# Kernel optimization log

Measured on AMD Instinct MI355X. Metric: run time of the kernel, lower is better.

The kernel has to match this reference:

```python
import jax, jax.numpy as jnp
import numpy as np

TEMPERATURE = 8.0


def setup_inputs() -> dict:
    key = jax.random.key(0)
    kq, kk, kv, kc = jax.random.split(key, 4)
    B, L, D = 4, 4096, 64
    q = jax.random.normal(kq, (B, L, D), dtype=jnp.float32)
    k = jax.random.normal(kk, (B, L, D), dtype=jnp.float32)
    v = jax.random.normal(kv, (B, L, D), dtype=jnp.float32)
    # vectors = stack(softmax(randn(d_v)), softmax(randn(d_v)))  (dim=0 softmax over d_v)
    raw = jax.random.normal(kc, (2, D), dtype=jnp.float32)
    vectors = jax.nn.softmax(raw, axis=1)
    return {"q": q, "k": k, "v": v, "vectors": vectors}


def reference(q, k, v, vectors):
    # Original builds diagonal core tensors cores[t,t,t] = vectors[.,t] for t < min(dimen, len_q),
    # then einsum('pqk,bip,bjq,bkr->bijr') and sums over j. With a diagonal core this collapses to:
    #   out[b,i,r] = sum_{t<m} q[b,i,t] * w[t] * ksum[b,t] * v[b,t,r]
    # where w = 0.5*(c1+c2)/temperature and ksum[b,t] = sum_j k[b,j,t].
    B, L, D = q.shape
    m = min(D, L)  # static python int
    w = 0.5 * (vectors[0, :m] + vectors[1, :m]) / TEMPERATURE          # [m]
    ksum = jnp.sum(k[:, :, :m], axis=1)                                 # [B, m]
    coef = w[None, :] * ksum                                            # [B, m]
    output = jnp.einsum('bit,bt,btr->bir', q[:, :, :m], coef, v[:, :m, :])  # [B, L, D]
    attn = jnp.einsum('bid,bjd->bij', q, k)                             # [B, L, L]
    return (output, attn)
```

## Files before the change

kernel.cpp:

```cpp
#include <hip/hip_runtime.h>
#include <stdint.h>

#define BB 4
#define LL 4096
#define DD 64

typedef __attribute__((ext_vector_type(8))) short bf16x8;
typedef __attribute__((ext_vector_type(4))) float f32x4;

static __device__ __forceinline__ unsigned short f2bf(float x) {
    unsigned int u = __builtin_bit_cast(unsigned int, x);
    u += 0x7fffu + ((u >> 16) & 1u);
    return (unsigned short)(u >> 16);
}

__global__ __launch_bounds__(256) void convert_kernel(
    const float* __restrict__ q, const float* __restrict__ k,
    unsigned short* __restrict__ qbf, unsigned short* __restrict__ kbf,
    float* __restrict__ part)
{
    const int NBQ = (BB * LL * DD) / 2048;
    int bid = blockIdx.x;
    bool is_k = bid >= NBQ;
    const float* src = is_k ? k : q;
    unsigned short* dst = is_k ? kbf : qbf;
    int cb = is_k ? (bid - NBQ) : bid;
    int tid = threadIdx.x;

    size_t idx0 = (size_t)cb * 2048 + (size_t)tid * 8;
    float4 f0 = *(const float4*)(src + idx0);
    float4 f1 = *(const float4*)(src + idx0 + 4);
    float f[8] = {f0.x, f0.y, f0.z, f0.w, f1.x, f1.y, f1.z, f1.w};

    unsigned short u[8];
    #pragma unroll
    for (int e = 0; e < 8; e++) u[e] = f2bf(f[e]);
    uint4 pk;
    pk.x = (unsigned)u[0] | ((unsigned)u[1] << 16);
    pk.y = (unsigned)u[2] | ((unsigned)u[3] << 16);
    pk.z = (unsigned)u[4] | ((unsigned)u[5] << 16);
    pk.w = (unsigned)u[6] | ((unsigned)u[7] << 16);
    *(uint4*)(dst + idx0) = pk;

    if (is_k) {
        __shared__ float red[256][8];
        #pragma unroll
        for (int e = 0; e < 8; e++) red[tid][e] = f[e];
        __syncthreads();
        if (tid < 64) {
            int g = tid >> 3, e = tid & 7;
            float s = 0.f;
            #pragma unroll
            for (int r = 0; r < 32; r++) s += red[r * 8 + g][e];
            part[(size_t)cb * 64 + tid] = s;
        }
    }
}

__global__ __launch_bounds__(256) void out_kernel(
    const float* __restrict__ q, const float* __restrict__ v,
    const float* __restrict__ vec, const float* __restrict__ part,
    float* __restrict__ out)
{
    __shared__ float csh[64];
    __shared__ float Vl[64][65];
    __shared__ float qs[32][65];

    int bid = blockIdx.x;
    int b   = bid >> 7;
    int i0  = (bid & 127) << 5;
    int tid = threadIdx.x;

    if (tid < 64) {
        const float* pp = part + (size_t)b * 128 * 64 + tid;
        float s = 0.f;
        #pragma unroll 8
        for (int c = 0; c < 128; c++) s += pp[c * 64];
        csh[tid] = 0.0625f * (vec[tid] + vec[64 + tid]) * s;
    }
    {
        const float* vb = v + (size_t)b * LL * DD;
        #pragma unroll
        for (int it = 0; it < 4; it++) {
            int idx4 = it * 256 + tid;
            int t  = idx4 >> 4;
            int r4 = (idx4 & 15) << 2;
            float4 w = *(const float4*)(vb + (size_t)idx4 * 4);
            Vl[t][r4 + 0] = w.x; Vl[t][r4 + 1] = w.y;
            Vl[t][r4 + 2] = w.z; Vl[t][r4 + 3] = w.w;
        }
    }
    __syncthreads();
    {
        const float* qb = q + (size_t)b * LL * DD;
        int row = tid >> 3;
        int t0  = (tid & 7) << 3;
        const float* src = qb + (size_t)(i0 + row) * DD + t0;
        float4 a0 = *(const float4*)(src);
        float4 a1 = *(const float4*)(src + 4);
        float fa[8] = {a0.x,a0.y,a0.z,a0.w,a1.x,a1.y,a1.z,a1.w};
        #pragma unroll
        for (int e = 0; e < 8; e++) qs[row][t0 + e] = fa[e] * csh[t0 + e];
    }
    __syncthreads();

    int ii = tid >> 3;
    int g  = tid & 7;
    float acc[8] = {0,0,0,0,0,0,0,0};
    #pragma unroll 8
    for (int t = 0; t < 64; t++) {
        float qv = qs[ii][t];
        #pragma unroll
        for (int j = 0; j < 8; j++) acc[j] += qv * Vl[t][g * 8 + j];
    }
    float* op = out + (size_t)b * LL * DD + (size_t)(i0 + ii) * DD + g * 8;
    float4 s0 = {acc[0], acc[1], acc[2], acc[3]};
    float4 s1 = {acc[4], acc[5], acc[6], acc[7]};
    *(float4*)(op)     = s0;
    *(float4*)(op + 4) = s1;
}

__global__ __launch_bounds__(256) void attn_kernel(
    const unsigned short* __restrict__ qbf,
    const unsigned short* __restrict__ kbf,
    float* __restrict__ attn)
{
    int bid = blockIdx.x;
    int swz = (bid & 7) * 512 + (bid >> 3);
    int b   = swz >> 10;
    int rem = swz & 1023;
    int ti  = rem >> 5;
    int tj  = rem & 31;

    int tid  = threadIdx.x;
    int wid  = tid >> 6;
    int lane = tid & 63;
    int wm = wid >> 1, wn = wid & 1;
    int row0 = ti * 128 + wm * 64;
    int col0 = tj * 128 + wn * 64;

    const unsigned short* qb = qbf + (size_t)b * LL * DD;
    const unsigned short* kb = kbf + (size_t)b * LL * DD;

    int lr = lane & 15;
    int lk = (lane >> 4) * 8;

    f32x4 acc[4][4];
    #pragma unroll
    for (int m = 0; m < 4; m++)
        #pragma unroll
        for (int n = 0; n < 4; n++)
            acc[m][n] = (f32x4){0.f, 0.f, 0.f, 0.f};

    #pragma unroll
    for (int kk = 0; kk < 2; kk++) {
        int k0 = kk * 32 + lk;
        bf16x8 qf[4], kf[4];
        #pragma unroll
        for (int m = 0; m < 4; m++)
            qf[m] = *(const bf16x8*)(qb + (size_t)(row0 + m * 16 + lr) * DD + k0);
        #pragma unroll
        for (int n = 0; n < 4; n++)
            kf[n] = *(const bf16x8*)(kb + (size_t)(col0 + n * 16 + lr) * DD + k0);
        #pragma unroll
        for (int m = 0; m < 4; m++)
            #pragma unroll
            for (int n = 0; n < 4; n++)
                acc[m][n] = __builtin_amdgcn_mfma_f32_16x16x32_bf16(
                    kf[n], qf[m], acc[m][n], 0, 0, 0);
    }

    float* ab = attn + (size_t)b * LL * LL;
    int jb = (lane >> 4) * 4;
    #pragma unroll
    for (int m = 0; m < 4; m++) {
        size_t roff = (size_t)(row0 + m * 16 + lr) * LL;
        #pragma unroll
        for (int n = 0; n < 4; n++) {
            *(f32x4*)(ab + roff + col0 + n * 16 + jb) = acc[m][n];
        }
    }
}

extern "C" void kernel_launch(void* const* d_in, const int* in_sizes, int n_in,
                              void* d_out, int out_size, void* d_ws, size_t ws_size,
                              hipStream_t stream) {
    const float* q   = (const float*)d_in[0];
    const float* k   = (const float*)d_in[1];
    const float* v   = (const float*)d_in[2];
    const float* vec = (const float*)d_in[3];

    float* out  = (float*)d_out;
    float* attn = out + (size_t)BB * LL * DD;

    unsigned short* qbf = (unsigned short*)d_ws;
    unsigned short* kbf = qbf + (size_t)BB * LL * DD;
    float* part = (float*)(kbf + (size_t)BB * LL * DD);

    convert_kernel<<<1024, 256, 0, stream>>>(q, k, qbf, kbf, part);
    out_kernel<<<512, 256, 0, stream>>>(q, v, vec, part, out);
    attn_kernel<<<4096, 256, 0, stream>>>(qbf, kbf, attn);
}
```

Measured before the change: 81.03 us.

## Stage attn tiles through swizzled LDS for fully coalesced row stores

The attn kernel now gives each block a 32x512 output tile instead of 128x128, with each wave computing 32x128. Results are written into an XOR-swizzled LDS buffer and then stored to global memory as contiguous 2KB row segments. Previously each lane wrote scattered 16-byte pieces across many rows. The aim is better write coalescing on the store-bound 256MB attn output, at the cost of 64KB of LDS per block, which limits occupancy, plus an extra LDS round trip and a barrier.

```diff
diff --git a/kernel.cpp b/kernel.cpp
--- a/kernel.cpp
+++ b/kernel.cpp
@@ -125,60 +125,74 @@
     const unsigned short* __restrict__ kbf,
     float* __restrict__ attn)
 {
+    __shared__ float lds[32 * 512];
+
     int bid = blockIdx.x;
     int swz = (bid & 7) * 512 + (bid >> 3);
     int b   = swz >> 10;
     int rem = swz & 1023;
-    int ti  = rem >> 5;
-    int tj  = rem & 31;
+    int ti  = rem >> 3;
+    int tj  = rem & 7;
 
     int tid  = threadIdx.x;
     int wid  = tid >> 6;
     int lane = tid & 63;
-    int wm = wid >> 1, wn = wid & 1;
-    int row0 = ti * 128 + wm * 64;
-    int col0 = tj * 128 + wn * 64;
+    int i0 = ti * 32;
+    int j0 = tj * 512;
+    int jw = j0 + wid * 128;
 
     const unsigned short* qb = qbf + (size_t)b * LL * DD;
     const unsigned short* kb = kbf + (size_t)b * LL * DD;
 
     int lr = lane & 15;
-    int lk = (lane >> 4) * 8;
-
-    f32x4 acc[4][4];
-    #pragma unroll
-    for (int m = 0; m < 4; m++)
-        #pragma unroll
-        for (int n = 0; n < 4; n++)
+    int g  = lane >> 4;
+    int lk = g * 8;
+
+    f32x4 acc[2][8];
+    #pragma unroll
+    for (int m = 0; m < 2; m++)
+        #pragma unroll
+        for (int n = 0; n < 8; n++)
             acc[m][n] = (f32x4){0.f, 0.f, 0.f, 0.f};
 
     #pragma unroll
     for (int kk = 0; kk < 2; kk++) {
         int k0 = kk * 32 + lk;
-        bf16x8 qf[4], kf[4];
-        #pragma unroll
-        for (int m = 0; m < 4; m++)
-            qf[m] = *(const bf16x8*)(qb + (size_t)(row0 + m * 16 + lr) * DD + k0);
-        #pragma unroll
-        for (int n = 0; n < 4; n++)
-            kf[n] = *(const bf16x8*)(kb + (size_t)(col0 + n * 16 + lr) * DD + k0);
-        #pragma unroll
-        for (int m = 0; m < 4; m++)
+        bf16x8 qf[2], kf[8];
+        #pragma unroll
+        for (int m = 0; m < 2; m++)
+            qf[m] = *(const bf16x8*)(qb + (size_t)(i0 + m * 16 + lr) * DD + k0);
+        #pragma unroll
+        for (int n = 0; n < 8; n++)
+            kf[n] = *(const bf16x8*)(kb + (size_t)(jw + n * 16 + lr) * DD + k0);
+        #pragma unroll
+        for (int m = 0; m < 2; m++)
             #pragma unroll
-            for (int n = 0; n < 4; n++)
+            for (int n = 0; n < 8; n++)
                 acc[m][n] = __builtin_amdgcn_mfma_f32_16x16x32_bf16(
                     kf[n], qf[m], acc[m][n], 0, 0, 0);
     }
 
+    f32x4* l4 = (f32x4*)lds;
+    #pragma unroll
+    for (int m = 0; m < 2; m++) {
+        int row = m * 16 + lr;
+        #pragma unroll
+        for (int n = 0; n < 8; n++) {
+            int col4 = wid * 32 + n * 4 + g;
+            l4[row * 128 + (col4 ^ (row & 7))] = acc[m][n];
+        }
+    }
+    __syncthreads();
+
     float* ab = attn + (size_t)b * LL * LL;
-    int jb = (lane >> 4) * 4;
-    #pragma unroll
-    for (int m = 0; m < 4; m++) {
-        size_t roff = (size_t)(row0 + m * 16 + lr) * LL;
-        #pragma unroll
-        for (int n = 0; n < 4; n++) {
-            *(f32x4*)(ab + roff + col0 + n * 16 + jb) = acc[m][n];
-        }
+    #pragma unroll
+    for (int it = 0; it < 16; it++) {
+        int flat4 = it * 256 + tid;
+        int row   = flat4 >> 7;
+        int col4  = flat4 & 127;
+        f32x4 v = l4[row * 128 + (col4 ^ (row & 7))];
+        *(f32x4*)(ab + (size_t)(i0 + row) * LL + j0 + col4 * 4) = v;
     }
 }
 
```

Result: faster. 78.47 us (-3.2%).
